# Kernel tuning notes

Hardware: AMD Instinct MI355X
Metric: run time of the kernel (lower is better)

## Reference

```python
import jax, jax.numpy as jnp
import numpy as np

EMBED = 1024
HEADS = 16
HEAD_DIM = EMBED // HEADS
RANK = 8
ALPHA = 16
SCALE_LORA = ALPHA / RANK  # 2.0


def _lora_linear(x, W, b, A, B):
    # F.linear(x, W, b) + scale * F.linear(F.linear(x, A), B)
    return x @ W.T + b + SCALE_LORA * ((x @ A.T) @ B.T)


def setup_inputs() -> dict:
    key = jax.random.key(0)
    ks = jax.random.split(key, 17)
    d = {"x": jax.random.normal(ks[0], (2, 2048, EMBED), dtype=jnp.float32)}
    names = ["q", "k", "v", "o"]
    i = 1
    for n in names:
        d[f"W{n}"] = jax.random.normal(ks[i], (EMBED, EMBED), dtype=jnp.float32) * 0.02; i += 1
        d[f"b{n}"] = jnp.zeros((EMBED,), dtype=jnp.float32)
        d[f"A{n}"] = jax.random.normal(ks[i], (RANK, EMBED), dtype=jnp.float32) * 0.02; i += 1
        d[f"B{n}"] = jax.random.normal(ks[i], (EMBED, RANK), dtype=jnp.float32) * 0.02; i += 1
    return d


def reference(x, Wq, bq, Aq, Bq, Wk, bk, Ak, Bk, Wv, bv, Av, Bv, Wo, bo, Ao, Bo):
    N, S, _ = x.shape
    Q = _lora_linear(x, Wq, bq, Aq, Bq).reshape(N, S, HEADS, HEAD_DIM)
    K = _lora_linear(x, Wk, bk, Ak, Bk).reshape(N, S, HEADS, HEAD_DIM)
    V = _lora_linear(x, Wv, bv, Av, Bv).reshape(N, S, HEADS, HEAD_DIM)
    # energy: [N, H, Sq, Sk]
    energy = jnp.einsum("nqhd,nkhd->nhqk", Q, K) / jnp.sqrt(jnp.float32(HEAD_DIM))
    attn = jax.nn.softmax(energy, axis=-1)
    out = jnp.einsum("nhqk,nkhd->nqhd", attn, V).reshape(N, S, EMBED)
    return _lora_linear(out, Wo, bo, Ao, Bo)
```

## Files before the change

kernel.cpp:

```cpp
#include <hip/hip_runtime.h>
#include <stdint.h>

typedef uint16_t u16;
typedef short s16x8 __attribute__((ext_vector_type(8)));
typedef float f32x4 __attribute__((ext_vector_type(4)));
typedef unsigned short u16x4 __attribute__((ext_vector_type(4)));
typedef uint32_t u32;
typedef u32 u32x2 __attribute__((ext_vector_type(2)));
typedef u32 u32x4 __attribute__((ext_vector_type(4)));

#define MFMA16(a,b,c) __builtin_amdgcn_mfma_f32_16x16x32_bf16((a),(b),(c),0,0,0)
#define QSCALE 0.18033688011112042f

__device__ __forceinline__ float b2f(u16 b){
  union { u32 u; float f; } v; v.u = ((u32)b)<<16; return v.f;
}
__device__ __forceinline__ u16 f2b(float f){
  union { float f; u32 u; } v; v.f = f;
  return (u16)((v.u + 0x7fffu + ((v.u>>16)&1u))>>16);
}
__device__ __forceinline__ u32 fbits(float f){
  union { float f; u32 u; } v; v.f = f; return v.u;
}
__device__ __forceinline__ float trunc_bf(float f){
  union { u32 u; float f; } v; v.u = fbits(f) & 0xffff0000u; return v.f;
}
__device__ __forceinline__ void load_lds_16B(const void* g, void* l){
  __builtin_amdgcn_global_load_lds((const __attribute__((address_space(1))) void*)g,
                                   (__attribute__((address_space(3))) void*)l, 16, 0, 0);
}

template<bool XF32, int NMAT>
__global__ __launch_bounds__(256) void lora_conv_kernel(
    const void* __restrict__ Xv,
    const float* __restrict__ A0, const float* __restrict__ A1, const float* __restrict__ A2,
    float* __restrict__ T0, float* __restrict__ T1, float* __restrict__ T2,
    u16* __restrict__ xb,
    const float* __restrict__ W0, const float* __restrict__ W1,
    const float* __restrict__ W2, const float* __restrict__ W3,
    u16* __restrict__ Wb)
{
  if (XF32 && blockIdx.x >= 1024){
    const int cv = blockIdx.x - 1024;
    const int y = cv>>8;
    const float* src = (y==0)?W0:(y==1)?W1:(y==2)?W2:W3;
    u16* dst = Wb + (size_t)y*1048576;
    const int g = (cv&255)*256 + threadIdx.x;
#pragma unroll
    for (int t=0;t<4;t++){
      const int i4 = g + t*65536;
      const f32x4 v = *(const f32x4*)(src + (size_t)i4*4);
      u16x4 o;
#pragma unroll
      for (int j=0;j<4;j++) o[j] = f2b(v[j]);
      *(u16x4*)(dst + (size_t)i4*4) = o;
    }
    return;
  }

  const int wid = threadIdx.x>>6, lane = threadIdx.x&63;
  const int m = blockIdx.x*4 + wid;

  float xf[16];
  if (XF32){
    const float* xp = (const float*)Xv + (size_t)m*1024 + lane*16;
#pragma unroll
    for (int q=0;q<4;q++){
      const f32x4 v = *(const f32x4*)(xp + q*4);
#pragma unroll
      for (int j=0;j<4;j++) xf[q*4+j] = v[j];
    }
    u16* xbp = xb + (size_t)m*1024 + lane*16;
#pragma unroll
    for (int q=0;q<4;q++){
      u16x4 o;
#pragma unroll
      for (int j=0;j<4;j++) o[j] = f2b(xf[q*4+j]);
      *(u16x4*)(xbp + q*4) = o;
    }
  } else {
    const u16* xp = (const u16*)Xv + (size_t)m*1024 + lane*16;
#pragma unroll
    for (int j=0;j<16;j++) xf[j] = b2f(xp[j]);
  }

#pragma unroll
  for (int mat=0; mat<NMAT; mat++){
    const float* A = (mat==0)?A0:(mat==1)?A1:A2;
    float* T = (mat==0)?T0:(mat==1)?T1:T2;
    float accv[8];
#pragma unroll
    for (int r=0;r<8;r++){
      const float* ap = A + r*1024 + lane*16;
      float s = 0.f;
#pragma unroll
      for (int q=0;q<4;q++){
        const f32x4 av = *(const f32x4*)(ap + q*4);
#pragma unroll
        for (int j=0;j<4;j++) s += xf[q*4+j]*av[j];
      }
      accv[r] = s;
    }
#pragma unroll
    for (int r=0;r<8;r++){
      float s = accv[r];
      s += __shfl_xor(s,1);  s += __shfl_xor(s,2);  s += __shfl_xor(s,4);
      s += __shfl_xor(s,8);  s += __shfl_xor(s,16); s += __shfl_xor(s,32);
      accv[r] = s;
    }
    if (lane==0){
#pragma unroll
      for (int r=0;r<8;r++) T[(size_t)m*8 + r] = accv[r];
    }
  }
}

__global__ __launch_bounds__(256,2) void gemm_qkv_kernel(
    const u16* __restrict__ Xb, const u16* __restrict__ Wb,
    const float* __restrict__ bq, const float* __restrict__ bk, const float* __restrict__ bv,
    const float* __restrict__ tq, const float* __restrict__ tk, const float* __restrict__ tv,
    const float* __restrict__ Blq, const float* __restrict__ Blk, const float* __restrict__ Blv,
    u16* __restrict__ Qb, u16* __restrict__ Kb, u16* __restrict__ Vtb)
{
  __shared__ u16 At[128*32];
  __shared__ u16 Bt[128*32];
  const int tid = threadIdx.x;
  const int wid = tid>>6, lane = tid&63;
  const int quad = lane>>4, l16 = lane&15;
  const int wm = wid>>1, wn = wid&1;
  const int proj = blockIdx.x>>3;
  const int n0 = (blockIdx.x&7)<<7, m0 = blockIdx.y<<7;
  const u16* W = Wb + (size_t)proj*1048576;
  const float* bias = (proj==0)?bq:(proj==1)?bk:bv;
  const float* T    = (proj==0)?tq:(proj==1)?tk:tv;
  const float* Bl   = (proj==0)?Blq:(proj==1)?Blk:Blv;
  const float scale = (proj==0)?QSCALE:1.0f;

  f32x4 acc[4][4];
#pragma unroll
  for (int i=0;i<4;i++)
#pragma unroll
    for (int j=0;j<4;j++) acc[i][j] = f32x4{0.f,0.f,0.f,0.f};

  for (int k0=0;k0<1024;k0+=32){
#pragma unroll
    for (int p=0;p<2;p++){
      const int s = wid*128 + p*64 + lane;
      const int row = s>>2, c = s&3;
      load_lds_16B(Xb + (size_t)(m0+row)*1024 + k0 + c*8, At + (wid*128+p*64)*8);
      load_lds_16B(W  + (size_t)(n0+row)*1024 + k0 + c*8, Bt + (wid*128+p*64)*8);
    }
    __syncthreads();
    s16x8 af[4], bfr[4];
#pragma unroll
    for (int t=0;t<4;t++){
      const int r = wm*64 + t*16 + l16;
      af[t]  = *(const s16x8*)(At + r*32 + quad*8);
      const int c = wn*64 + t*16 + l16;
      bfr[t] = *(const s16x8*)(Bt + c*32 + quad*8);
    }
#pragma unroll
    for (int tm=0;tm<4;tm++)
#pragma unroll
      for (int tn=0;tn<4;tn++)
        acc[tm][tn] = MFMA16(af[tm], bfr[tn], acc[tm][tn]);
    __syncthreads();
  }

  s16x8 tf[4], bfl[4];
#pragma unroll
  for (int t=0;t<4;t++){ tf[t] = s16x8{0,0,0,0,0,0,0,0}; bfl[t] = s16x8{0,0,0,0,0,0,0,0}; }
  if (quad==0){
#pragma unroll
    for (int tm=0;tm<4;tm++){
      const float* tp = T + (size_t)(m0 + wm*64 + tm*16 + l16)*8;
      const f32x4 a0 = *(const f32x4*)(tp);
      const f32x4 a1 = *(const f32x4*)(tp+4);
#pragma unroll
      for (int j=0;j<4;j++){ tf[tm][j] = (short)f2b(2.0f*a0[j]); tf[tm][4+j] = (short)f2b(2.0f*a1[j]); }
    }
#pragma unroll
    for (int tn=0;tn<4;tn++){
      const float* bp = Bl + (size_t)(n0 + wn*64 + tn*16 + l16)*8;
      const f32x4 b0 = *(const f32x4*)(bp);
      const f32x4 b1 = *(const f32x4*)(bp+4);
#pragma unroll
      for (int j=0;j<4;j++){ bfl[tn][j] = (short)f2b(b0[j]); bfl[tn][4+j] = (short)f2b(b1[j]); }
    }
  }
#pragma unroll
  for (int tm=0;tm<4;tm++)
#pragma unroll
    for (int tn=0;tn<4;tn++)
      acc[tm][tn] = MFMA16(tf[tm], bfl[tn], acc[tm][tn]);

#pragma unroll
  for (int tn=0;tn<4;tn++){
    const int n = n0 + wn*64 + tn*16 + l16;
    const float bn = bias[n];
#pragma unroll
    for (int tm=0;tm<4;tm++){
      const int mb = m0 + wm*64 + tm*16 + quad*4;
      if (proj==0){
#pragma unroll
        for (int rg=0;rg<4;rg++) Qb[(size_t)(mb+rg)*1024 + n] = f2b((acc[tm][tn][rg]+bn)*scale);
      } else if (proj==1){
#pragma unroll
        for (int rg=0;rg<4;rg++) Kb[(size_t)(mb+rg)*1024 + n] = f2b(acc[tm][tn][rg]+bn);
      } else {
        const int batch = mb>>11, sI = mb&2047;
        const int hh = n>>6, dd = n&63;
        u16x4 pk;
#pragma unroll
        for (int rg=0;rg<4;rg++) pk[rg] = f2b(acc[tm][tn][rg]+bn);
        *(u16x4*)(Vtb + (size_t)((batch*16+hh)*64+dd)*2048 + sI) = pk;
      }
    }
  }
}

__global__ __launch_bounds__(256,2) void gemm_o_kernel(
    const u16* __restrict__ Xb, const u16* __restrict__ W,
    const float* __restrict__ bias, const float* __restrict__ T,
    const float* __restrict__ Bl, float* __restrict__ Out)
{
  __shared__ u16 At[128*32];
  __shared__ u16 Bt[64*32];
  const int tid = threadIdx.x;
  const int wid = tid>>6, lane = tid&63;
  const int quad = lane>>4, l16 = lane&15;
  const int wm = wid>>1, wn = wid&1;
  const int m0 = blockIdx.y<<7, n0 = blockIdx.x<<6;

  f32x4 acc[4][2];
#pragma unroll
  for (int i=0;i<4;i++)
#pragma unroll
    for (int j=0;j<2;j++) acc[i][j] = f32x4{0.f,0.f,0.f,0.f};

  for (int k0=0;k0<1024;k0+=32){
#pragma unroll
    for (int p=0;p<2;p++){
      const int s = wid*128 + p*64 + lane;
      const int row = s>>2, c = s&3;
      load_lds_16B(Xb + (size_t)(m0+row)*1024 + k0 + c*8, At + (wid*128+p*64)*8);
    }
    { const int s = wid*64 + lane;
      const int row = s>>2, c = s&3;
      load_lds_16B(W + (size_t)(n0+row)*1024 + k0 + c*8, Bt + (wid*64)*8); }
    __syncthreads();
    s16x8 af[4], bfr[2];
#pragma unroll
    for (int t=0;t<4;t++){
      const int r = wm*64 + t*16 + l16;
      af[t] = *(const s16x8*)(At + r*32 + quad*8);
    }
#pragma unroll
    for (int t=0;t<2;t++){
      const int c = wn*32 + t*16 + l16;
      bfr[t] = *(const s16x8*)(Bt + c*32 + quad*8);
    }
#pragma unroll
    for (int tm=0;tm<4;tm++)
#pragma unroll
      for (int tn=0;tn<2;tn++)
        acc[tm][tn] = MFMA16(af[tm], bfr[tn], acc[tm][tn]);
    __syncthreads();
  }

  s16x8 tf[4], bfl[2];
#pragma unroll
  for (int t=0;t<4;t++) tf[t] = s16x8{0,0,0,0,0,0,0,0};
#pragma unroll
  for (int t=0;t<2;t++) bfl[t] = s16x8{0,0,0,0,0,0,0,0};
  if (quad==0){
#pragma unroll
    for (int tm=0;tm<4;tm++){
      const float* tp = T + (size_t)(m0 + wm*64 + tm*16 + l16)*8;
      const f32x4 a0 = *(const f32x4*)(tp);
      const f32x4 a1 = *(const f32x4*)(tp+4);
#pragma unroll
      for (int j=0;j<4;j++){ tf[tm][j] = (short)f2b(2.0f*a0[j]); tf[tm][4+j] = (short)f2b(2.0f*a1[j]); }
    }
#pragma unroll
    for (int tn=0;tn<2;tn++){
      const float* bp = Bl + (size_t)(n0 + wn*32 + tn*16 + l16)*8;
      const f32x4 b0 = *(const f32x4*)(bp);
      const f32x4 b1 = *(const f32x4*)(bp+4);
#pragma unroll
      for (int j=0;j<4;j++){ bfl[tn][j] = (short)f2b(b0[j]); bfl[tn][4+j] = (short)f2b(b1[j]); }
    }
  }
#pragma unroll
  for (int tm=0;tm<4;tm++)
#pragma unroll
    for (int tn=0;tn<2;tn++)
      acc[tm][tn] = MFMA16(tf[tm], bfl[tn], acc[tm][tn]);

#pragma unroll
  for (int tn=0;tn<2;tn++){
    const int n = n0 + wn*32 + tn*16 + l16;
    const float bn = bias[n];
#pragma unroll
    for (int tm=0;tm<4;tm++){
      const int mb = m0 + wm*64 + tm*16 + quad*4;
#pragma unroll
      for (int rg=0;rg<4;rg++)
        Out[(size_t)(mb+rg)*1024 + n] = acc[tm][tn][rg] + bn;
    }
  }
}

__global__ __launch_bounds__(256,2) void attn_kernel(
    const u16* __restrict__ Q, const u16* __restrict__ K,
    const u16* __restrict__ Vt, u16* __restrict__ Out)
{
  __shared__ u16 KtB[2][128*72];
  __shared__ u16 VtB[2][64*136];
  const int tid = threadIdx.x;
  const int wid = tid>>6, lane = tid&63;
  const int quad = lane>>4, l16 = lane&15;
  const int q0 = blockIdx.x<<7;
  const int h = blockIdx.y, nb = blockIdx.z;
  const int qw = wid*32;

  s16x8 qf[2][2];
#pragma unroll
  for (int g=0;g<2;g++){
    const int row = q0 + qw + g*16 + l16;
#pragma unroll
    for (int dh=0;dh<2;dh++)
      qf[g][dh] = *(const s16x8*)(Q + (size_t)(nb*2048+row)*1024 + h*64 + dh*32 + quad*8);
  }
  f32x4 OT[2][4];
  float lr[2] = {0.f, 0.f};
#pragma unroll
  for (int g=0;g<2;g++)
#pragma unroll
    for (int td=0;td<4;td++) OT[g][td] = f32x4{0.f,0.f,0.f,0.f};

  s16x8 kreg[4], vreg[4];
  auto LOADT = [&](int kn){
#pragma unroll
    for (int p=0;p<4;p++){
      const int s = p*256 + tid;
      kreg[p] = *(const s16x8*)(K + (size_t)(nb*2048+kn+(s>>3))*1024 + h*64 + (s&7)*8);
      vreg[p] = *(const s16x8*)(Vt + (size_t)((nb*16+h)*64+(s>>4))*2048 + kn + (s&15)*8);
    }
  };
  auto WRITET = [&](int b){
    u16* Ktb = KtB[b]; u16* Vtb = VtB[b];
#pragma unroll
    for (int p=0;p<4;p++){
      const int s = p*256 + tid;
      *(s16x8*)(Ktb + (s>>3)*72 + (s&7)*8) = kreg[p];
      *(s16x8*)(Vtb + (s>>4)*136 + (s&15)*8) = vreg[p];
    }
  };

  LOADT(0);
  WRITET(0);
  LOADT(128);
  __syncthreads();

  for (int t=0;t<16;t++){
    const int cur = t&1;
    if (t < 15) WRITET(cur^1);
    if (t < 14) LOADT((t+2)*128);
    const u16* KtC = KtB[cur];
    const u16* VtC = VtB[cur];

#pragma unroll
    for (int kb=0;kb<4;kb++){
      u32 ew[2][2], ow[2][2];
#pragma unroll
      for (int sel=0;sel<2;sel++){
        const int key = (kb*2+sel)*16 + l16;
        const s16x8 kf0 = *(const s16x8*)(KtC + key*72 + quad*8);
        const s16x8 kf1 = *(const s16x8*)(KtC + key*72 + 32 + quad*8);
#pragma unroll
        for (int g=0;g<2;g++){
          f32x4 z = f32x4{0.f,0.f,0.f,0.f};
          z = MFMA16(kf0, qf[g][0], z);
          z = MFMA16(kf1, qf[g][1], z);
          const float p0 = __builtin_amdgcn_exp2f(z[0]);
          const float p1 = __builtin_amdgcn_exp2f(z[1]);
          const float p2 = __builtin_amdgcn_exp2f(z[2]);
          const float p3 = __builtin_amdgcn_exp2f(z[3]);
          lr[g] += (trunc_bf(p0)+trunc_bf(p1)) + (trunc_bf(p2)+trunc_bf(p3));
          const u32 w0 = __builtin_amdgcn_perm(fbits(p1), fbits(p0), 0x07060302u);
          const u32 w1 = __builtin_amdgcn_perm(fbits(p3), fbits(p2), 0x07060302u);
          if (sel==0){ ew[g][0]=w0; ew[g][1]=w1; } else { ow[g][0]=w0; ow[g][1]=w1; }
        }
      }
      s16x8 pf[2];
#pragma unroll
      for (int g=0;g<2;g++){
        const u32x2 r32 = __builtin_amdgcn_permlane32_swap(ew[g][0], ow[g][0], false, false);
        const u32x2 r16 = __builtin_amdgcn_permlane16_swap(r32[0], r32[1], false, false);
        const u32x2 s32 = __builtin_amdgcn_permlane32_swap(ew[g][1], ow[g][1], false, false);
        const u32x2 s16v = __builtin_amdgcn_permlane16_swap(s32[0], s32[1], false, false);
        u32x4 pw; pw[0]=r16[0]; pw[1]=s16v[0]; pw[2]=r16[1]; pw[3]=s16v[1];
        pf[g] = __builtin_bit_cast(s16x8, pw);
      }
      __builtin_amdgcn_s_setprio(1);
#pragma unroll
      for (int td=0;td<4;td++){
        const s16x8 vf = *(const s16x8*)(VtC + (td*16+l16)*136 + kb*32 + quad*8);
#pragma unroll
        for (int g=0;g<2;g++)
          OT[g][td] = MFMA16(vf, pf[g], OT[g][td]);
      }
      __builtin_amdgcn_s_setprio(0);
    }
    __syncthreads();
  }

#pragma unroll
  for (int g=0;g<2;g++){
    float t = lr[g];
    t += __shfl_xor(t,16);
    t += __shfl_xor(t,32);
    const float linv = 1.0f / t;
    const int q = q0 + qw + g*16 + l16;
#pragma unroll
    for (int td=0;td<4;td++){
      u16x4 pk;
#pragma unroll
      for (int rg=0;rg<4;rg++) pk[rg] = f2b(OT[g][td][rg]*linv);
      *(u16x4*)(Out + (size_t)(nb*2048+q)*1024 + h*64 + td*16 + quad*4) = pk;
    }
  }
}

extern "C" void kernel_launch(void* const* d_in, const int* in_sizes, int n_in,
                              void* d_out, int out_size, void* d_ws, size_t ws_size,
                              hipStream_t stream)
{
  const float* x  = (const float*)d_in[0];
  const float* Wq = (const float*)d_in[1];  const float* bq = (const float*)d_in[2];
  const float* Aq = (const float*)d_in[3];  const float* Bq = (const float*)d_in[4];
  const float* Wk = (const float*)d_in[5];  const float* bk = (const float*)d_in[6];
  const float* Ak = (const float*)d_in[7];  const float* Bk = (const float*)d_in[8];
  const float* Wv = (const float*)d_in[9];  const float* bv = (const float*)d_in[10];
  const float* Av = (const float*)d_in[11]; const float* Bv = (const float*)d_in[12];
  const float* Wo = (const float*)d_in[13]; const float* bo = (const float*)d_in[14];
  const float* Ao = (const float*)d_in[15]; const float* Bo = (const float*)d_in[16];

  char* ws = (char*)d_ws;
  float* tq = (float*)(ws + 0);
  float* tk = (float*)(ws + 131072);
  float* tv = (float*)(ws + 262144);
  float* to = (float*)(ws + 393216);
  u16* xb  = (u16*)(ws + 524288);
  u16* Ab  = xb;
  u16* Wb  = (u16*)(ws + 524288 + 8388608);
  u16* Qb  = (u16*)(ws + 524288 + 2*8388608);
  u16* Kb  = (u16*)(ws + 524288 + 3*8388608);
  u16* Vtb = (u16*)(ws + 524288 + 4*8388608);

  lora_conv_kernel<true,3><<<dim3(2048),256,0,stream>>>(
      x, Aq, Ak, Av, tq, tk, tv, xb, Wq, Wk, Wv, Wo, Wb);
  gemm_qkv_kernel<<<dim3(24,32),256,0,stream>>>(xb, Wb, bq, bk, bv, tq, tk, tv,
                                                Bq, Bk, Bv, Qb, Kb, Vtb);
  attn_kernel<<<dim3(16,16,2),256,0,stream>>>(Qb, Kb, Vtb, Ab);
  lora_conv_kernel<false,1><<<dim3(1024),256,0,stream>>>(
      Ab, Ao, Ao, Ao, to, to, to, nullptr,
      nullptr, nullptr, nullptr, nullptr, nullptr);
  gemm_o_kernel<<<dim3(16,32),256,0,stream>>>(Ab, Wb + (size_t)3*1048576, bo, to, Bo,
                                              (float*)d_out);
}
```

Measured before the change: 242.7 us.

## Split attention key range across wave pairs and compute row sums via MFMA

```diff
diff --git a/kernel.cpp b/kernel.cpp
--- a/kernel.cpp
+++ b/kernel.cpp
@@ -21,9 +21,6 @@
 }
 __device__ __forceinline__ u32 fbits(float f){
   union { float f; u32 u; } v; v.f = f; return v.u;
-}
-__device__ __forceinline__ float trunc_bf(float f){
-  union { u32 u; float f; } v; v.u = fbits(f) & 0xffff0000u; return v.f;
 }
 __device__ __forceinline__ void load_lds_16B(const void* g, void* l){
   __builtin_amdgcn_global_load_lds((const __attribute__((address_space(1))) void*)g,
@@ -311,7 +308,7 @@
   }
 }
 
-__global__ __launch_bounds__(256,2) void attn_kernel(
+__global__ __launch_bounds__(512,4) void attn_kernel(
     const u16* __restrict__ Q, const u16* __restrict__ K,
     const u16* __restrict__ Vt, u16* __restrict__ Out)
 {
@@ -322,7 +319,9 @@
   const int quad = lane>>4, l16 = lane&15;
   const int q0 = blockIdx.x<<7;
   const int h = blockIdx.y, nb = blockIdx.z;
-  const int qw = wid*32;
+  const int qg = wid>>1;
+  const int kh = wid&1;
+  const int qw = qg*32;
 
   s16x8 qf[2][2];
 #pragma unroll
@@ -333,17 +332,22 @@
       qf[g][dh] = *(const s16x8*)(Q + (size_t)(nb*2048+row)*1024 + h*64 + dh*32 + quad*8);
   }
   f32x4 OT[2][4];
-  float lr[2] = {0.f, 0.f};
-#pragma unroll
-  for (int g=0;g<2;g++)
+  f32x4 Lacc[2];
+#pragma unroll
+  for (int g=0;g<2;g++){
 #pragma unroll
     for (int td=0;td<4;td++) OT[g][td] = f32x4{0.f,0.f,0.f,0.f};
-
-  s16x8 kreg[4], vreg[4];
+    Lacc[g] = f32x4{0.f,0.f,0.f,0.f};
+  }
+  s16x8 ones;
+#pragma unroll
+  for (int j=0;j<8;j++) ones[j] = (short)0x3F80;
+
+  s16x8 kreg[2], vreg[2];
   auto LOADT = [&](int kn){
 #pragma unroll
-    for (int p=0;p<4;p++){
-      const int s = p*256 + tid;
+    for (int p=0;p<2;p++){
+      const int s = p*512 + tid;
       kreg[p] = *(const s16x8*)(K + (size_t)(nb*2048+kn+(s>>3))*1024 + h*64 + (s&7)*8);
       vreg[p] = *(const s16x8*)(Vt + (size_t)((nb*16+h)*64+(s>>4))*2048 + kn + (s&15)*8);
     }
@@ -351,8 +355,8 @@
   auto WRITET = [&](int b){
     u16* Ktb = KtB[b]; u16* Vtb = VtB[b];
 #pragma unroll
-    for (int p=0;p<4;p++){
-      const int s = p*256 + tid;
+    for (int p=0;p<2;p++){
+      const int s = p*512 + tid;
       *(s16x8*)(Ktb + (s>>3)*72 + (s&7)*8) = kreg[p];
       *(s16x8*)(Vtb + (s>>4)*136 + (s&15)*8) = vreg[p];
     }
@@ -371,11 +375,11 @@
     const u16* VtC = VtB[cur];
 
 #pragma unroll
-    for (int kb=0;kb<4;kb++){
+    for (int kb=0;kb<2;kb++){
       u32 ew[2][2], ow[2][2];
 #pragma unroll
       for (int sel=0;sel<2;sel++){
-        const int key = (kb*2+sel)*16 + l16;
+        const int key = kh*64 + kb*32 + sel*16 + l16;
         const s16x8 kf0 = *(const s16x8*)(KtC + key*72 + quad*8);
         const s16x8 kf1 = *(const s16x8*)(KtC + key*72 + 32 + quad*8);
 #pragma unroll
@@ -387,7 +391,6 @@
           const float p1 = __builtin_amdgcn_exp2f(z[1]);
           const float p2 = __builtin_amdgcn_exp2f(z[2]);
           const float p3 = __builtin_amdgcn_exp2f(z[3]);
-          lr[g] += (trunc_bf(p0)+trunc_bf(p1)) + (trunc_bf(p2)+trunc_bf(p3));
           const u32 w0 = __builtin_amdgcn_perm(fbits(p1), fbits(p0), 0x07060302u);
           const u32 w1 = __builtin_amdgcn_perm(fbits(p3), fbits(p2), 0x07060302u);
           if (sel==0){ ew[g][0]=w0; ew[g][1]=w1; } else { ow[g][0]=w0; ow[g][1]=w1; }
@@ -406,29 +409,46 @@
       __builtin_amdgcn_s_setprio(1);
 #pragma unroll
       for (int td=0;td<4;td++){
-        const s16x8 vf = *(const s16x8*)(VtC + (td*16+l16)*136 + kb*32 + quad*8);
+        const s16x8 vf = *(const s16x8*)(VtC + (td*16+l16)*136 + kh*64 + kb*32 + quad*8);
 #pragma unroll
         for (int g=0;g<2;g++)
           OT[g][td] = MFMA16(vf, pf[g], OT[g][td]);
       }
+#pragma unroll
+      for (int g=0;g<2;g++)
+        Lacc[g] = MFMA16(ones, pf[g], Lacc[g]);
       __builtin_amdgcn_s_setprio(0);
     }
     __syncthreads();
   }
 
-#pragma unroll
-  for (int g=0;g<2;g++){
-    float t = lr[g];
-    t += __shfl_xor(t,16);
-    t += __shfl_xor(t,32);
-    const float linv = 1.0f / t;
-    const int q = q0 + qw + g*16 + l16;
-#pragma unroll
-    for (int td=0;td<4;td++){
-      u16x4 pk;
-#pragma unroll
-      for (int rg=0;rg<4;rg++) pk[rg] = f2b(OT[g][td][rg]*linv);
-      *(u16x4*)(Out + (size_t)(nb*2048+q)*1024 + h*64 + td*16 + quad*4) = pk;
+  float* ep = (float*)KtB;
+  float* lw = (float*)VtB;
+  if (kh==1){
+#pragma unroll
+    for (int g=0;g<2;g++){
+      const int q = qw + g*16 + l16;
+#pragma unroll
+      for (int td=0;td<4;td++)
+        *(f32x4*)(ep + q*68 + td*16 + quad*4) = OT[g][td];
+      if (quad==0) lw[q] = Lacc[g][0];
+    }
+  }
+  __syncthreads();
+  if (kh==0){
+#pragma unroll
+    for (int g=0;g<2;g++){
+      const int q = qw + g*16 + l16;
+      const float linv = 1.0f / (Lacc[g][0] + lw[q]);
+      const int qout = q0 + q;
+#pragma unroll
+      for (int td=0;td<4;td++){
+        const f32x4 o2 = *(const f32x4*)(ep + q*68 + td*16 + quad*4);
+        u16x4 pk;
+#pragma unroll
+        for (int rg=0;rg<4;rg++) pk[rg] = f2b((OT[g][td][rg]+o2[rg])*linv);
+        *(u16x4*)(Out + (size_t)(nb*2048+qout)*1024 + h*64 + td*16 + quad*4) = pk;
+      }
     }
   }
 }
@@ -463,7 +483,7 @@
       x, Aq, Ak, Av, tq, tk, tv, xb, Wq, Wk, Wv, Wo, Wb);
   gemm_qkv_kernel<<<dim3(24,32),256,0,stream>>>(xb, Wb, bq, bk, bv, tq, tk, tv,
                                                 Bq, Bk, Bv, Qb, Kb, Vtb);
-  attn_kernel<<<dim3(16,16,2),256,0,stream>>>(Qb, Kb, Vtb, Ab);
+  attn_kernel<<<dim3(16,16,2),512,0,stream>>>(Qb, Kb, Vtb, Ab);
   lora_conv_kernel<false,1><<<dim3(1024),256,0,stream>>>(
       Ab, Ao, Ao, Ao, to, to, to, nullptr,
       nullptr, nullptr, nullptr, nullptr, nullptr);
```

Result: no change. 238.6 us (-1.7%).
